# Kernel optimization log

Measured on AMD Instinct MI355X. Metric: run time of the kernel, lower is better.

The kernel has to match this reference:

```python
import jax, jax.numpy as jnp
import numpy as np

B, N, C, H = 2, 2048, 1024, 16
HD = C // H  # head dim = 64


def setup_inputs() -> dict:
    key = jax.random.key(0)
    kq, kk, kv, km = jax.random.split(key, 4)
    q = jax.random.normal(kq, (B, N, C), dtype=jnp.float32)
    k = jax.random.normal(kk, (B, N, C), dtype=jnp.float32)
    v = jax.random.normal(kv, (B, N, C), dtype=jnp.float32)
    mask = jax.random.randint(km, (B, 1, N, N), 0, 2, dtype=jnp.int32)
    return {"q": q, "k": k, "v": v, "mask": mask}


def reference(q, k, v, mask):
    b, n, c = q.shape
    # (B, N, C) -> (B, H, N, HD)
    qh = q.reshape(b, n, H, HD).transpose(0, 2, 1, 3)
    kh = k.reshape(b, n, H, HD).transpose(0, 2, 1, 3)
    vh = v.reshape(b, n, H, HD).transpose(0, 2, 1, 3)
    scale = 1.0 / jnp.sqrt(jnp.float32(HD))
    # scores: (B, H, N, N)
    scores = jnp.einsum("bhqd,bhkd->bhqk", qh, kh) * scale
    scores = jnp.where(mask == 0, jnp.float32(-1e9), scores)
    probs = jax.nn.softmax(scores, axis=-1)
    atten = jnp.einsum("bhqk,bhkd->bhqd", probs, vh)
    # (B, H, N, HD) -> (B, N, C)
    return atten.transpose(0, 2, 1, 3).reshape(b, n, c)
```

## Files before the change

### kernel.cpp

```cpp
#include <hip/hip_runtime.h>
#include <hip/hip_bf16.h>

#define B_ 2
#define N_ 2048
#define C_ 1024
#define H_ 16
#define HD_ 64

#define KT 64
#define NT (N_ / KT)
#define KSTR 72
#define VSTR 72
#define PSTR 72
#define NW 8
#define QB 128

typedef short s16x8 __attribute__((ext_vector_type(8)));
typedef short s16x4 __attribute__((ext_vector_type(4)));
typedef float f32x4 __attribute__((ext_vector_type(4)));

__device__ __forceinline__ s16x8 cvt8(float4 a, float4 b) {
    union { s16x8 v; __hip_bfloat162 h[4]; } u;
    u.h[0] = __float22bfloat162_rn(float2{a.x, a.y});
    u.h[1] = __float22bfloat162_rn(float2{a.z, a.w});
    u.h[2] = __float22bfloat162_rn(float2{b.x, b.y});
    u.h[3] = __float22bfloat162_rn(float2{b.z, b.w});
    return u.v;
}

__global__ __launch_bounds__(256)
void pack_mask(const int* __restrict__ M, unsigned long long* __restrict__ bits) {
    const int gw   = (blockIdx.x * 256 + threadIdx.x) >> 6;
    const int lane = threadIdx.x & 63;
#pragma unroll
    for (int it = 0; it < 16; ++it) {
        const size_t wi = (size_t)gw * 16 + it;
        unsigned long long bal = __ballot(M[wi * 64 + lane] != 0);
        if (lane == 0) bits[wi] = bal;
    }
}

__global__ __launch_bounds__(512, 4)
void mha_fwd(const float* __restrict__ Q, const float* __restrict__ K,
             const float* __restrict__ V, const unsigned* __restrict__ bits,
             float* __restrict__ O) {
    __shared__ ushort Kl[2][KT * KSTR];
    __shared__ ushort Vt[2][HD_ * VSTR];
    __shared__ ushort Pl[NW][16 * PSTR];

    const int qt   = blockIdx.x;
    const int h    = blockIdx.y;
    const int b    = blockIdx.z;
    const int tid  = threadIdx.x;
    const int w    = tid >> 6;
    const int lane = tid & 63;
    const int l16  = lane & 15;
    const int quad = lane >> 4;

    const size_t head_off = (size_t)b * N_ * C_ + (size_t)h * HD_;
    const int qb = qt * QB + w * 16;

    const float qs = 0.125f * 1.44269504088896f;
    const size_t qoff = head_off + (size_t)(qb + l16) * C_ + quad * 8;
    float4 q0 = *(const float4*)(Q + qoff);
    float4 q1 = *(const float4*)(Q + qoff + 4);
    float4 q2 = *(const float4*)(Q + qoff + 32);
    float4 q3 = *(const float4*)(Q + qoff + 36);
    q0.x*=qs; q0.y*=qs; q0.z*=qs; q0.w*=qs;
    q1.x*=qs; q1.y*=qs; q1.z*=qs; q1.w*=qs;
    q2.x*=qs; q2.y*=qs; q2.z*=qs; q2.w*=qs;
    q3.x*=qs; q3.y*=qs; q3.z*=qs; q3.w*=qs;
    const s16x8 qa0 = cvt8(q0, q1);
    const s16x8 qa1 = cvt8(q2, q3);

    f32x4 acc[4];
#pragma unroll
    for (int c = 0; c < 4; ++c) acc[c] = f32x4{0.f, 0.f, 0.f, 0.f};
    float lsum = 0.f;

    const int skey = tid >> 3;
    const int sd0  = (tid & 7) * 8;
    const int kp   = tid >> 4;
    const int vd0  = (tid & 15) * 4;
    const int vcol = 2 * (kp & 3) + ((((kp >> 2) ^ (vd0 >> 3)) & 7) << 3);

    const unsigned* brow = bits + ((size_t)b * N_ + qb + l16) * (N_ / 32);

    const float SHIFT = 16.0f;

    {
        const size_t kbase = head_off + (size_t)(skey) * C_ + sd0;
        float4 kA = *(const float4*)(K + kbase);
        float4 kB = *(const float4*)(K + kbase + 4);
        *(s16x8*)(&Kl[0][skey * KSTR + sd0]) = cvt8(kA, kB);
        const size_t vbase = head_off + (size_t)(2 * kp) * C_ + vd0;
        float4 vA = *(const float4*)(V + vbase);
        float4 vB = *(const float4*)(V + vbase + C_);
        const float* ap = (const float*)&vA;
        const float* bp = (const float*)&vB;
#pragma unroll
        for (int i = 0; i < 4; ++i) {
            __hip_bfloat162 pr = __float22bfloat162_rn(float2{ap[i], bp[i]});
            *(unsigned*)(&Vt[0][(vd0 + i) * VSTR + vcol]) = *(unsigned*)&pr;
        }
    }

    for (int kt = 0; kt < NT; ++kt) {
        const int cur = kt & 1;
        float4 kA, kB, vA, vB;
        const bool has_next = (kt + 1 < NT);
        if (has_next) {
            const size_t kbase = head_off + (size_t)((kt + 1) * KT + skey) * C_ + sd0;
            kA = *(const float4*)(K + kbase);
            kB = *(const float4*)(K + kbase + 4);
            const size_t vbase = head_off + (size_t)((kt + 1) * KT + 2 * kp) * C_ + vd0;
            vA = *(const float4*)(V + vbase);
            vB = *(const float4*)(V + vbase + C_);
        }
        const unsigned w0 = brow[2 * kt];
        const unsigned w1 = brow[2 * kt + 1];

        __syncthreads();

        f32x4 s[4];
#pragma unroll
        for (int t = 0; t < 4; ++t) {
            s16x8 kb0 = *(const s16x8*)(&Kl[cur][(t * 16 + l16) * KSTR + quad * 8]);
            s16x8 kb1 = *(const s16x8*)(&Kl[cur][(t * 16 + l16) * KSTR + quad * 8 + 32]);
            f32x4 z = {0.f, 0.f, 0.f, 0.f};
            z = __builtin_amdgcn_mfma_f32_16x16x32_bf16(kb0, qa0, z, 0, 0, 0);
            z = __builtin_amdgcn_mfma_f32_16x16x32_bf16(kb1, qa1, z, 0, 0, 0);
            s[t] = z;
        }

        const unsigned a0 = w0 >> (quad * 4);
        const unsigned a1 = w1 >> (quad * 4);
#pragma unroll
        for (int t = 0; t < 4; ++t) {
            const unsigned aw = (t < 2) ? a0 : a1;
            const int sh = (t & 1) * 16;
            float p0 = exp2f((((aw >> (sh + 0)) & 1u) ? s[t][0] : -1e9f) - SHIFT);
            float p1 = exp2f((((aw >> (sh + 1)) & 1u) ? s[t][1] : -1e9f) - SHIFT);
            float p2 = exp2f((((aw >> (sh + 2)) & 1u) ? s[t][2] : -1e9f) - SHIFT);
            float p3 = exp2f((((aw >> (sh + 3)) & 1u) ? s[t][3] : -1e9f) - SHIFT);
            lsum += (p0 + p1) + (p2 + p3);
            union { s16x4 v; __hip_bfloat162 h[2]; } u;
            u.h[0] = __float22bfloat162_rn(float2{p0, p1});
            u.h[1] = __float22bfloat162_rn(float2{p2, p3});
            *(s16x4*)(&Pl[w][l16 * PSTR + t * 16 + quad * 4]) = u.v;
        }

#pragma unroll
        for (int half = 0; half < 2; ++half) {
            s16x8 pa = *(const s16x8*)(&Pl[w][l16 * PSTR + half * 32 + quad * 8]);
#pragma unroll
            for (int c = 0; c < 4; ++c) {
                const int dr  = c * 16 + l16;
                const int blk = (half * 4 + quad) ^ ((dr >> 3) & 7);
                s16x8 vb = *(const s16x8*)(&Vt[cur][dr * VSTR + blk * 8]);
                acc[c] = __builtin_amdgcn_mfma_f32_16x16x32_bf16(pa, vb, acc[c], 0, 0, 0);
            }
        }

        if (has_next) {
            *(s16x8*)(&Kl[1 - cur][skey * KSTR + sd0]) = cvt8(kA, kB);
            const float* ap = (const float*)&vA;
            const float* bp = (const float*)&vB;
#pragma unroll
            for (int i = 0; i < 4; ++i) {
                __hip_bfloat162 pr = __float22bfloat162_rn(float2{ap[i], bp[i]});
                *(unsigned*)(&Vt[1 - cur][(vd0 + i) * VSTR + vcol]) = *(unsigned*)&pr;
            }
        }
    }

    lsum += __shfl_xor(lsum, 16);
    lsum += __shfl_xor(lsum, 32);

#pragma unroll
    for (int r = 0; r < 4; ++r) {
        const float inv = 1.0f / __shfl(lsum, quad * 4 + r);
        const size_t obase = head_off + (size_t)(qb + quad * 4 + r) * C_;
        O[obase + l16]      = acc[0][r] * inv;
        O[obase + l16 + 16] = acc[1][r] * inv;
        O[obase + l16 + 32] = acc[2][r] * inv;
        O[obase + l16 + 48] = acc[3][r] * inv;
    }
}

extern "C" void kernel_launch(void* const* d_in, const int* in_sizes, int n_in,
                              void* d_out, int out_size, void* d_ws, size_t ws_size,
                              hipStream_t stream) {
    const float* q = (const float*)d_in[0];
    const float* k = (const float*)d_in[1];
    const float* v = (const float*)d_in[2];
    const int*   m = (const int*)d_in[3];
    float*       o = (float*)d_out;

    hipLaunchKernelGGL(pack_mask, dim3(2048), dim3(256), 0, stream,
                       m, (unsigned long long*)d_ws);

    dim3 grid(N_ / QB, H_, B_);
    hipLaunchKernelGGL(mha_fwd, grid, dim3(512), 0, stream,
                       q, k, v, (const unsigned*)d_ws, o);
}
```

Measured before the change: 195.0 us.

## Pre-convert K/V to swizzled bf16 tiles and stream them via global_load_lds

Adds two pre-pass kernels that convert K and V from fp32 to bf16 once, laid out as per-tile swizzled 64x64 blocks (V transposed) in workspace. The attention kernel then copies each tile straight into LDS with async global_load_lds, so it no longer re-reads fp32 K/V and converts them in every query block. It also drops the constant exp2 shift. This cuts the repeated global traffic and conversion work (16 query tiles each reread K/V), at the cost of two extra launches plus a workspace write and read. The old path is kept as a fallback when the workspace is too small.

Measured after the change: 193.0 us. Within noise of the previous version (-1.0%).

```diff
diff --git a/kernel.cpp b/kernel.cpp
--- a/kernel.cpp
+++ b/kernel.cpp
@@ -9,8 +9,7 @@
 
 #define KT 64
 #define NT (N_ / KT)
-#define KSTR 72
-#define VSTR 72
+#define TILE_E 4096
 #define PSTR 72
 #define NW 8
 #define QB 128
@@ -18,6 +17,11 @@
 typedef short s16x8 __attribute__((ext_vector_type(8)));
 typedef short s16x4 __attribute__((ext_vector_type(4)));
 typedef float f32x4 __attribute__((ext_vector_type(4)));
+
+__device__ __forceinline__ ushort f2bf(float x) {
+    __hip_bfloat16 h = __float2bfloat16(x);
+    return *reinterpret_cast<ushort*>(&h);
+}
 
 __device__ __forceinline__ s16x8 cvt8(float4 a, float4 b) {
     union { s16x8 v; __hip_bfloat162 h[4]; } u;
@@ -28,6 +32,12 @@
     return u.v;
 }
 
+__device__ __forceinline__ void gll16(const void* g, void* l) {
+    __builtin_amdgcn_global_load_lds(
+        (const __attribute__((address_space(1))) unsigned*)g,
+        (__attribute__((address_space(3))) unsigned*)l, 16, 0, 0);
+}
+
 __global__ __launch_bounds__(256)
 void pack_mask(const int* __restrict__ M, unsigned long long* __restrict__ bits) {
     const int gw   = (blockIdx.x * 256 + threadIdx.x) >> 6;
@@ -40,12 +50,55 @@
     }
 }
 
+__global__ __launch_bounds__(256)
+void conv_k(const float* __restrict__ K, ushort* __restrict__ Kw) {
+    const int gt = blockIdx.x * 256 + threadIdx.x;
+    const int b  = gt >> 18;
+    const int h  = (gt >> 14) & 15;
+    const int n  = (gt >> 3) & 2047;
+    const int db = gt & 7;
+    const size_t src = (size_t)(b * N_ + n) * C_ + h * 64 + db * 8;
+    float4 f0 = *(const float4*)(K + src);
+    float4 f1 = *(const float4*)(K + src + 4);
+    const int key = n & 63, kt = n >> 6;
+    ushort* dst = Kw + (size_t)((b * H_ + h) * NT + kt) * TILE_E
+                     + key * 64 + ((db ^ (key & 7)) * 8);
+    *(s16x8*)dst = cvt8(f0, f1);
+}
+
+__global__ __launch_bounds__(256)
+void conv_v(const float* __restrict__ V, ushort* __restrict__ Vw) {
+    const int gt  = blockIdx.x * 256 + threadIdx.x;
+    const int b   = gt >> 16;
+    const int h   = (gt >> 12) & 15;
+    const int kt  = (gt >> 7) & 31;
+    const int kb4 = (gt >> 3) & 15;
+    const int db  = gt & 7;
+    const int key0 = kb4 * 4;
+    float f[4][8];
+#pragma unroll
+    for (int i = 0; i < 4; ++i) {
+        const size_t src = (size_t)(b * N_ + kt * 64 + key0 + i) * C_ + h * 64 + db * 8;
+        *(float4*)&f[i][0] = *(const float4*)(V + src);
+        *(float4*)&f[i][4] = *(const float4*)(V + src + 4);
+    }
+    ushort* tb = Vw + (size_t)((b * H_ + h) * NT + kt) * TILE_E;
+#pragma unroll
+    for (int j = 0; j < 8; ++j) {
+        const int d = db * 8 + j;
+        union { s16x4 v; __hip_bfloat162 h2[2]; } u;
+        u.h2[0] = __float22bfloat162_rn(float2{f[0][j], f[1][j]});
+        u.h2[1] = __float22bfloat162_rn(float2{f[2][j], f[3][j]});
+        *(s16x4*)(tb + d * 64 + (((key0 >> 3) ^ (d & 7)) * 8) + (key0 & 7)) = u.v;
+    }
+}
+
 __global__ __launch_bounds__(512, 4)
-void mha_fwd(const float* __restrict__ Q, const float* __restrict__ K,
-             const float* __restrict__ V, const unsigned* __restrict__ bits,
+void mha_fwd(const float* __restrict__ Q, const ushort* __restrict__ Kw,
+             const ushort* __restrict__ Vw, const unsigned* __restrict__ bits,
              float* __restrict__ O) {
-    __shared__ ushort Kl[2][KT * KSTR];
-    __shared__ ushort Vt[2][HD_ * VSTR];
+    __shared__ ushort Kl[2][TILE_E];
+    __shared__ ushort Vt[2][TILE_E];
     __shared__ ushort Pl[NW][16 * PSTR];
 
     const int qt   = blockIdx.x;
@@ -78,18 +131,116 @@
     for (int c = 0; c < 4; ++c) acc[c] = f32x4{0.f, 0.f, 0.f, 0.f};
     float lsum = 0.f;
 
-    const int skey = tid >> 3;
-    const int sd0  = (tid & 7) * 8;
-    const int kp   = tid >> 4;
-    const int vd0  = (tid & 15) * 4;
+    const size_t tilebase = (size_t)((b * H_ + h) * NT) * TILE_E;
+    const ushort* Kg = Kw + tilebase + (size_t)tid * 8;
+    const ushort* Vg = Vw + tilebase + (size_t)tid * 8;
+
+    const unsigned* brow = bits + ((size_t)b * N_ + qb + l16) * (N_ / 32);
+
+    gll16(Kg, &Kl[0][w * 512]);
+    gll16(Vg, &Vt[0][w * 512]);
+
+    for (int kt = 0; kt < NT; ++kt) {
+        const int cur = kt & 1;
+        __syncthreads();
+        if (kt + 1 < NT) {
+            gll16(Kg + (size_t)(kt + 1) * TILE_E, &Kl[1 - cur][w * 512]);
+            gll16(Vg + (size_t)(kt + 1) * TILE_E, &Vt[1 - cur][w * 512]);
+        }
+        const unsigned w0 = brow[2 * kt];
+        const unsigned w1 = brow[2 * kt + 1];
+
+        f32x4 s[4];
+#pragma unroll
+        for (int t = 0; t < 4; ++t) {
+            const int key = t * 16 + l16;
+            s16x8 kb0 = *(const s16x8*)(&Kl[cur][key * 64 + ((quad ^ (key & 7)) * 8)]);
+            s16x8 kb1 = *(const s16x8*)(&Kl[cur][key * 64 + (((4 + quad) ^ (key & 7)) * 8)]);
+            f32x4 z = {0.f, 0.f, 0.f, 0.f};
+            z = __builtin_amdgcn_mfma_f32_16x16x32_bf16(kb0, qa0, z, 0, 0, 0);
+            z = __builtin_amdgcn_mfma_f32_16x16x32_bf16(kb1, qa1, z, 0, 0, 0);
+            s[t] = z;
+        }
+
+        const unsigned a0 = w0 >> (quad * 4);
+        const unsigned a1 = w1 >> (quad * 4);
+#pragma unroll
+        for (int t = 0; t < 4; ++t) {
+            const unsigned aw = (t < 2) ? a0 : a1;
+            const int sh = (t & 1) * 16;
+            float p0 = exp2f(((aw >> (sh + 0)) & 1u) ? s[t][0] : -1e9f);
+            float p1 = exp2f(((aw >> (sh + 1)) & 1u) ? s[t][1] : -1e9f);
+            float p2 = exp2f(((aw >> (sh + 2)) & 1u) ? s[t][2] : -1e9f);
+            float p3 = exp2f(((aw >> (sh + 3)) & 1u) ? s[t][3] : -1e9f);
+            lsum += (p0 + p1) + (p2 + p3);
+            union { s16x4 v; __hip_bfloat162 h2[2]; } u;
+            u.h2[0] = __float22bfloat162_rn(float2{p0, p1});
+            u.h2[1] = __float22bfloat162_rn(float2{p2, p3});
+            *(s16x4*)(&Pl[w][l16 * PSTR + t * 16 + quad * 4]) = u.v;
+        }
+
+#pragma unroll
+        for (int half = 0; half < 2; ++half) {
+            s16x8 pa = *(const s16x8*)(&Pl[w][l16 * PSTR + half * 32 + quad * 8]);
+#pragma unroll
+            for (int c = 0; c < 4; ++c) {
+                const int dr = c * 16 + l16;
+                s16x8 vb = *(const s16x8*)(&Vt[cur][dr * 64 + (((half * 4 + quad) ^ (dr & 7)) * 8)]);
+                acc[c] = __builtin_amdgcn_mfma_f32_16x16x32_bf16(pa, vb, acc[c], 0, 0, 0);
+            }
+        }
+    }
+
+    lsum += __shfl_xor(lsum, 16);
+    lsum += __shfl_xor(lsum, 32);
+
+#pragma unroll
+    for (int r = 0; r < 4; ++r) {
+        const float inv = 1.0f / __shfl(lsum, quad * 4 + r);
+        const size_t obase = head_off + (size_t)(qb + quad * 4 + r) * C_;
+        O[obase + l16]      = acc[0][r] * inv;
+        O[obase + l16 + 16] = acc[1][r] * inv;
+        O[obase + l16 + 32] = acc[2][r] * inv;
+        O[obase + l16 + 48] = acc[3][r] * inv;
+    }
+}
+
+#define KSTR 72
+#define VSTR 72
+__global__ __launch_bounds__(512, 4)
+void mha_fwd_fb(const float* __restrict__ Q, const float* __restrict__ K,
+                const float* __restrict__ V, const unsigned* __restrict__ bits,
+                float* __restrict__ O) {
+    __shared__ ushort Kl[2][KT * KSTR];
+    __shared__ ushort Vt[2][HD_ * VSTR];
+    __shared__ ushort Pl[NW][16 * PSTR];
+    const int qt = blockIdx.x, h = blockIdx.y, b = blockIdx.z, tid = threadIdx.x;
+    const int w = tid >> 6, lane = tid & 63, l16 = lane & 15, quad = lane >> 4;
+    const size_t head_off = (size_t)b * N_ * C_ + (size_t)h * HD_;
+    const int qb = qt * QB + w * 16;
+    const float qs = 0.125f * 1.44269504088896f;
+    const size_t qoff = head_off + (size_t)(qb + l16) * C_ + quad * 8;
+    float4 q0 = *(const float4*)(Q + qoff);
+    float4 q1 = *(const float4*)(Q + qoff + 4);
+    float4 q2 = *(const float4*)(Q + qoff + 32);
+    float4 q3 = *(const float4*)(Q + qoff + 36);
+    q0.x*=qs; q0.y*=qs; q0.z*=qs; q0.w*=qs;
+    q1.x*=qs; q1.y*=qs; q1.z*=qs; q1.w*=qs;
+    q2.x*=qs; q2.y*=qs; q2.z*=qs; q2.w*=qs;
+    q3.x*=qs; q3.y*=qs; q3.z*=qs; q3.w*=qs;
+    const s16x8 qa0 = cvt8(q0, q1);
+    const s16x8 qa1 = cvt8(q2, q3);
+    f32x4 acc[4];
+#pragma unroll
+    for (int c = 0; c < 4; ++c) acc[c] = f32x4{0.f, 0.f, 0.f, 0.f};
+    float lsum = 0.f;
+    const int skey = tid >> 3, sd0 = (tid & 7) * 8;
+    const int kp = tid >> 4, vd0 = (tid & 15) * 4;
     const int vcol = 2 * (kp & 3) + ((((kp >> 2) ^ (vd0 >> 3)) & 7) << 3);
-
     const unsigned* brow = bits + ((size_t)b * N_ + qb + l16) * (N_ / 32);
-
     const float SHIFT = 16.0f;
-
     {
-        const size_t kbase = head_off + (size_t)(skey) * C_ + sd0;
+        const size_t kbase = head_off + (size_t)skey * C_ + sd0;
         float4 kA = *(const float4*)(K + kbase);
         float4 kB = *(const float4*)(K + kbase + 4);
         *(s16x8*)(&Kl[0][skey * KSTR + sd0]) = cvt8(kA, kB);
@@ -104,7 +255,6 @@
             *(unsigned*)(&Vt[0][(vd0 + i) * VSTR + vcol]) = *(unsigned*)&pr;
         }
     }
-
     for (int kt = 0; kt < NT; ++kt) {
         const int cur = kt & 1;
         float4 kA, kB, vA, vB;
@@ -119,9 +269,7 @@
         }
         const unsigned w0 = brow[2 * kt];
         const unsigned w1 = brow[2 * kt + 1];
-
         __syncthreads();
-
         f32x4 s[4];
 #pragma unroll
         for (int t = 0; t < 4; ++t) {
@@ -132,7 +280,6 @@
             z = __builtin_amdgcn_mfma_f32_16x16x32_bf16(kb1, qa1, z, 0, 0, 0);
             s[t] = z;
         }
-
         const unsigned a0 = w0 >> (quad * 4);
         const unsigned a1 = w1 >> (quad * 4);
 #pragma unroll
@@ -144,24 +291,22 @@
             float p2 = exp2f((((aw >> (sh + 2)) & 1u) ? s[t][2] : -1e9f) - SHIFT);
             float p3 = exp2f((((aw >> (sh + 3)) & 1u) ? s[t][3] : -1e9f) - SHIFT);
             lsum += (p0 + p1) + (p2 + p3);
-            union { s16x4 v; __hip_bfloat162 h[2]; } u;
-            u.h[0] = __float22bfloat162_rn(float2{p0, p1});
-            u.h[1] = __float22bfloat162_rn(float2{p2, p3});
+            union { s16x4 v; __hip_bfloat162 h2[2]; } u;
+            u.h2[0] = __float22bfloat162_rn(float2{p0, p1});
+            u.h2[1] = __float22bfloat162_rn(float2{p2, p3});
             *(s16x4*)(&Pl[w][l16 * PSTR + t * 16 + quad * 4]) = u.v;
         }
-
 #pragma unroll
         for (int half = 0; half < 2; ++half) {
             s16x8 pa = *(const s16x8*)(&Pl[w][l16 * PSTR + half * 32 + quad * 8]);
 #pragma unroll
             for (int c = 0; c < 4; ++c) {
-                const int dr  = c * 16 + l16;
+                const int dr = c * 16 + l16;
                 const int blk = (half * 4 + quad) ^ ((dr >> 3) & 7);
                 s16x8 vb = *(const s16x8*)(&Vt[cur][dr * VSTR + blk * 8]);
                 acc[c] = __builtin_amdgcn_mfma_f32_16x16x32_bf16(pa, vb, acc[c], 0, 0, 0);
             }
         }
-
         if (has_next) {
             *(s16x8*)(&Kl[1 - cur][skey * KSTR + sd0]) = cvt8(kA, kB);
             const float* ap = (const float*)&vA;
@@ -173,10 +318,8 @@
             }
         }
     }
-
     lsum += __shfl_xor(lsum, 16);
     lsum += __shfl_xor(lsum, 32);
-
 #pragma unroll
     for (int r = 0; r < 4; ++r) {
         const float inv = 1.0f / __shfl(lsum, quad * 4 + r);
@@ -197,10 +340,23 @@
     const int*   m = (const int*)d_in[3];
     float*       o = (float*)d_out;
 
-    hipLaunchKernelGGL(pack_mask, dim3(2048), dim3(256), 0, stream,
-                       m, (unsigned long long*)d_ws);
+    const size_t BITS_BYTES = (size_t)B_ * N_ * N_ / 8;
+    const size_t KV_BYTES   = (size_t)B_ * H_ * N_ * HD_ * 2;
+    const size_t NEED       = BITS_BYTES + 2 * KV_BYTES;
+
+    unsigned long long* bits = (unsigned long long*)d_ws;
+    hipLaunchKernelGGL(pack_mask, dim3(2048), dim3(256), 0, stream, m, bits);
 
     dim3 grid(N_ / QB, H_, B_);
-    hipLaunchKernelGGL(mha_fwd, grid, dim3(512), 0, stream,
-                       q, k, v, (const unsigned*)d_ws, o);
-}
+    if (ws_size >= NEED) {
+        ushort* kw = (ushort*)((char*)d_ws + BITS_BYTES);
+        ushort* vw = (ushort*)((char*)d_ws + BITS_BYTES + KV_BYTES);
+        hipLaunchKernelGGL(conv_k, dim3(2048), dim3(256), 0, stream, k, kw);
+        hipLaunchKernelGGL(conv_v, dim3(512), dim3(256), 0, stream, v, vw);
+        hipLaunchKernelGGL(mha_fwd, grid, dim3(512), 0, stream,
+                           q, kw, vw, (const unsigned*)bits, o);
+    } else {
+        hipLaunchKernelGGL(mha_fwd_fb, grid, dim3(512), 0, stream,
+                           q, k, v, (const unsigned*)bits, o);
+    }
+}
```
